# Optimization experiments

Measured on AMD Instinct MI355X. Metric: run time of the kernel, lower is better.

Reference implementation:

```python
import jax, jax.numpy as jnp
import numpy as np

B, T, D, H, K, V, L = 512, 80, 540, 6, 90, 30522, 6  # batch, ctx, d_model, heads, head_size, vocab, blocks


def _layernorm(x, g, b, eps=1e-5):
    m = jnp.mean(x, axis=-1, keepdims=True)
    v = jnp.mean(jnp.square(x - m), axis=-1, keepdims=True)
    return (x - m) * jax.lax.rsqrt(v + eps) * g + b


def setup_inputs() -> dict:
    key = jax.random.key(0)
    ks = jax.random.split(key, 12)
    s = 0.02
    return {
        "x_batch": jax.random.randint(ks[0], (B, T), 0, V),
        "embed": jax.random.normal(ks[1], (V, D), jnp.float32) * s,
        "pos_embed": jax.random.normal(ks[2], (T, D), jnp.float32) * s,
        # per-block stacked per-head projection weights, applied as x @ W
        "Wq": jax.random.normal(ks[3], (L, H, D, K), jnp.float32) * s,
        "Wk": jax.random.normal(ks[4], (L, H, D, K), jnp.float32) * s,
        "Wv": jax.random.normal(ks[5], (L, H, D, K), jnp.float32) * s,
        "W1": jax.random.normal(ks[6], (L, D, H * K), jnp.float32) * s,
        "b1": jnp.zeros((L, H * K), jnp.float32),
        "W2": jax.random.normal(ks[7], (L, H * K, D), jnp.float32) * s,
        "b2": jnp.zeros((L, D), jnp.float32),
        "ln1_g": jnp.ones((L, D), jnp.float32),
        "ln1_b": jnp.zeros((L, D), jnp.float32),
        "ln2_g": jnp.ones((L, D), jnp.float32),
        "ln2_b": jnp.zeros((L, D), jnp.float32),
        "Wc": jax.random.normal(ks[8], (T * D, 1), jnp.float32) * s,
        "bc": jnp.zeros((1,), jnp.float32),
    }


def reference(x_batch, embed, pos_embed, Wq, Wk, Wv, W1, b1, W2, b2,
              ln1_g, ln1_b, ln2_g, ln2_b, Wc, bc):
    x = embed[x_batch] + pos_embed[jnp.arange(x_batch.shape[1])]  # [B,T,D]
    scale = K ** -0.5
    for i in range(L):
        q = jnp.einsum('btd,hdk->bhtk', x, Wq[i])
        k = jnp.einsum('btd,hdk->bhtk', x, Wk[i])
        v = jnp.einsum('btd,hdk->bhtk', x, Wv[i])
        scores = jnp.einsum('btk,bsk->bts'.replace('b', 'bh'), q, k) * scale  # [B,H,T,T]
        # original: Softmax(dim=1) on [B,T,T] -> normalize over the QUERY axis
        attn = jax.nn.softmax(scores, axis=2)
        o = jnp.einsum('bhts,bhsk->bhtk', attn, v)
        o = o.transpose(0, 2, 1, 3).reshape(x.shape)  # concat heads -> [B,T,D]
        x = _layernorm(o + x, ln1_g[i], ln1_b[i])
        ff = jax.nn.relu(x @ W1[i] + b1[i]) @ W2[i] + b2[i]
        x = _layernorm(ff + x, ln2_g[i], ln2_b[i])
    flat = x.reshape(x.shape[0], -1)  # [B, T*D]
    return flat @ Wc + bc  # [B,1]
```

## Files before the change

kernel.cpp:

```cpp
#include <hip/hip_runtime.h>
#include <hip/hip_bf16.h>
#include <math.h>

typedef __hip_bfloat16 bf16;
typedef __bf16 bf16x8 __attribute__((ext_vector_type(8)));
typedef __bf16 bf16x4 __attribute__((ext_vector_type(4)));
typedef float floatx4 __attribute__((ext_vector_type(4)));

#define BB 512
#define TT 80
#define DD 540
#define HH 6
#define KK 90
#define LL 6
#define HK 540
#define N3 1620
#define BT 40960
#define TD 43200
#define KP2 576
#define NQ 1664
#define NQ2 1792
#define NF 640
#define NF2 768
#define TP 104
#define NKT 9

__device__ inline float toF(bf16 x) { return __bfloat162float(x); }


__global__ void prep_wqkv(const float* __restrict__ Wq,
                          const float* __restrict__ Wk,
                          const float* __restrict__ Wv,
                          bf16* __restrict__ wTt) {
    int idx = blockIdx.x * blockDim.x + threadIdx.x;
    const int total = LL * NQ2 * KP2;
    if (idx >= total) return;
    int k = idx % KP2;
    int n = (idx / KP2) % NQ2;
    int l = idx / (KP2 * NQ2);
    float v = 0.f;
    if (k < DD && n < N3) {
        int sel = n / HK;
        int nn = n - sel * HK;
        int h = nn / KK, kk = nn - h * KK;
        const float* W = (sel == 0) ? Wq : ((sel == 1) ? Wk : Wv);
        v = W[(((size_t)l * HH + h) * DD + k) * KK + kk];
    }
    wTt[idx] = __float2bfloat16(v);
}

__global__ void prep_wt(const float* __restrict__ W, bf16* __restrict__ Wt) {
    int idx = blockIdx.x * blockDim.x + threadIdx.x;
    const int total = LL * NF2 * KP2;
    if (idx >= total) return;
    int k = idx % KP2;
    int n = (idx / KP2) % NF2;
    int l = idx / (KP2 * NF2);
    float v = 0.f;
    if (k < DD && n < DD)
        v = W[((size_t)l * DD + k) * DD + n];
    Wt[idx] = __float2bfloat16(v);
}

__global__ void embed_kernel(const int* __restrict__ ids,
                             const float* __restrict__ embed,
                             const float* __restrict__ pos,
                             bf16* __restrict__ xc, int rows) {
    int idx = blockIdx.x * blockDim.x + threadIdx.x;
    int total = rows * KP2;
    if (idx >= total) return;
    int d = idx % KP2;
    int bt = idx / KP2;
    float v = 0.f;
    if (d < DD) {
        int t = bt % TT;
        v = embed[(size_t)ids[bt] * DD + d] + pos[t * DD + d];
    }
    xc[idx] = __float2bfloat16(v);
}


__device__ inline void stage_pair(const bf16* __restrict__ Ab, int lda,
                                  const bf16* __restrict__ Bb,
                                  bf16* ldsbuf, int k0, int wave, int lane,
                                  const int jbase) {
    const int plane = wave >> 1;
    const int kh = plane & 1;
    const bf16* src = (plane < 2) ? Ab : Bb;
    const int ld = (plane < 2) ? lda : KP2;
    const int sc = (lane & 3) ^ ((lane >> 3) & 3);
    const int rsub = lane >> 2;
    bf16* pl = ldsbuf + plane * 8192;
#pragma unroll
    for (int jj = 0; jj < 2; ++jj) {
        int rg = (wave & 1) * 8 + jbase + jj;
        int row = rg * 16 + rsub;
        __builtin_amdgcn_global_load_lds(
            (const __attribute__((address_space(1))) void*)(src + (size_t)row * ld + k0 + kh * 32 + sc * 8),
            (__attribute__((address_space(3))) void*)(pl + rg * 512 + lane * 8), 16, 0, 0);
    }
}

#define READ_A(dst, buf, mh)                                                    \
    _Pragma("unroll")                                                           \
    for (int i_ = 0; i_ < 4; ++i_) {                                            \
        _Pragma("unroll")                                                       \
        for (int kh_ = 0; kh_ < 2; ++kh_) {                                     \
            int row_ = wr * 128 + (4 * (mh) + i_) * 16 + r;                     \
            dst[i_ * 2 + kh_] = *(const bf16x8*)((buf) + kh_ * 8192 + row_ * 32 + ksw); \
        }                                                                       \
    }

#define READ_B(dst, buf, nh)                                                    \
    _Pragma("unroll")                                                           \
    for (int j_ = 0; j_ < 2; ++j_) {                                            \
        _Pragma("unroll")                                                       \
        for (int kh_ = 0; kh_ < 2; ++kh_) {                                     \
            int row_ = wc * 64 + (2 * (nh) + j_) * 16 + r;                      \
            dst[j_ * 2 + kh_] = *(const bf16x8*)((buf) + 16384 + kh_ * 8192 + row_ * 32 + ksw); \
        }                                                                       \
    }

#define MFMA_Q(mh, av, bv, nh)                                                  \
    _Pragma("unroll")                                                           \
    for (int i_ = 0; i_ < 4; ++i_)                                              \
        _Pragma("unroll")                                                       \
        for (int j_ = 0; j_ < 2; ++j_)                                          \
            _Pragma("unroll")                                                   \
            for (int kh_ = 0; kh_ < 2; ++kh_)                                   \
                acc[4 * (mh) + i_][2 * (nh) + j_] =                             \
                    __builtin_amdgcn_mfma_f32_16x16x32_bf16(                    \
                        av[i_ * 2 + kh_], bv[j_ * 2 + kh_],                     \
                        acc[4 * (mh) + i_][2 * (nh) + j_], 0, 0, 0);

#define PHASE_MID                                                               \
    __builtin_amdgcn_s_barrier();                                               \
    asm volatile("s_waitcnt lgkmcnt(0)" ::: "memory");                          \
    __builtin_amdgcn_sched_barrier(0);

#define PHASE_TAIL                                                              \
    __builtin_amdgcn_sched_barrier(0);                                          \
    __builtin_amdgcn_s_barrier();                                               \
    __builtin_amdgcn_sched_barrier(0);

__global__ __launch_bounds__(512, 2) void mfma_gemm2(
    const bf16* __restrict__ A, int lda,
    const bf16* __restrict__ Bt,
    bf16* __restrict__ C, int ldc, int Nreal,
    const float* __restrict__ bias, int relu)
{
    extern __shared__ __align__(16) bf16 ldsb[];
    const int tid = threadIdx.x;
    const int lane = tid & 63;
    const int wave = tid >> 6;
    const int wr = wave >> 2;
    const int wc = wave & 3;
    const int q = lane >> 4, r = lane & 15;

    int bx = blockIdx.x, by = blockIdx.y;
    {
        int nwg = gridDim.x * gridDim.y;
        if ((nwg & 7) == 0) {
            int orig = by * gridDim.x + bx;
            int per = nwg >> 3;
            int swz = (orig & 7) * per + (orig >> 3);
            bx = swz % gridDim.x;
            by = swz / gridDim.x;
        }
    }
    const int row0 = by * 256;
    const int col0 = bx * 256;

    floatx4 acc[8][4];
#pragma unroll
    for (int i = 0; i < 8; ++i)
#pragma unroll
        for (int j = 0; j < 4; ++j) acc[i][j] = (floatx4){0.f, 0.f, 0.f, 0.f};

    const bf16* Ab = A + (size_t)row0 * lda;
    const bf16* Bb = Bt + (size_t)col0 * KP2;

    const int ksw = (q ^ ((r >> 1) & 3)) * 8;

    stage_pair(Ab, lda, Bb, ldsb, 0, wave, lane, 0);
    stage_pair(Ab, lda, Bb, ldsb, 0, wave, lane, 2);
    stage_pair(Ab, lda, Bb, ldsb, 0, wave, lane, 4);
    stage_pair(Ab, lda, Bb, ldsb, 0, wave, lane, 6);
    asm volatile("s_waitcnt vmcnt(0)" ::: "memory");
    __builtin_amdgcn_s_barrier();
    __builtin_amdgcn_sched_barrier(0);

    for (int kt = 0; kt < NKT; ++kt) {
        bf16* buf = ldsb + (kt & 1) * 32768;
        bf16* sbuf = ldsb + ((kt + 1) & 1) * 32768;
        const int k1 = (kt + 1) * 64;
        const bool st = (kt + 1 < NKT);

        bf16x8 a0[8], a1[8], b0[4], b1[4];

        READ_A(a0, buf, 0);
        READ_B(b0, buf, 0);
        if (st) stage_pair(Ab, lda, Bb, sbuf, k1, wave, lane, 0);
        PHASE_MID
        __builtin_amdgcn_s_setprio(1);
        MFMA_Q(0, a0, b0, 0);
        __builtin_amdgcn_s_setprio(0);
        PHASE_TAIL

        READ_A(a1, buf, 1);
        if (st) stage_pair(Ab, lda, Bb, sbuf, k1, wave, lane, 2);
        PHASE_MID
        __builtin_amdgcn_s_setprio(1);
        MFMA_Q(1, a1, b0, 0);
        __builtin_amdgcn_s_setprio(0);
        PHASE_TAIL

        READ_B(b1, buf, 1);
        if (st) stage_pair(Ab, lda, Bb, sbuf, k1, wave, lane, 4);
        PHASE_MID
        __builtin_amdgcn_s_setprio(1);
        MFMA_Q(0, a0, b1, 1);
        __builtin_amdgcn_s_setprio(0);
        PHASE_TAIL

        if (st) stage_pair(Ab, lda, Bb, sbuf, k1, wave, lane, 6);
        PHASE_MID
        __builtin_amdgcn_s_setprio(1);
        MFMA_Q(1, a1, b1, 1);
        __builtin_amdgcn_s_setprio(0);
        asm volatile("s_waitcnt vmcnt(0)" ::: "memory");
        PHASE_TAIL
    }

#pragma unroll
    for (int mi = 0; mi < 8; ++mi) {
        int m0 = row0 + wr * 128 + mi * 16 + q * 4;
#pragma unroll
        for (int ni = 0; ni < 4; ++ni) {
            int n = col0 + wc * 64 + ni * 16 + r;
            if (n < ldc) {
                bool valid = (n < Nreal);
                float bv = (valid && bias) ? bias[n] : 0.f;
#pragma unroll
                for (int reg = 0; reg < 4; ++reg) {
                    float v = acc[mi][ni][reg] + bv;
                    if (relu) v = fmaxf(v, 0.f);
                    if (!valid) v = 0.f;
                    C[(size_t)(m0 + reg) * ldc + n] = __float2bfloat16(v);
                }
            }
        }
    }
}

__global__ __launch_bounds__(320) void attn_mfma(const bf16* __restrict__ qkv,
                                                 bf16* __restrict__ obuf) {
    extern __shared__ bf16 lds[];
    bf16* Qs = lds;
    bf16* Ks = lds + 80 * TP;
    bf16* Vt = lds + 160 * TP;
    const int b = blockIdx.x / HH, h = blockIdx.x % HH;
    const int tid = threadIdx.x;
    const int lane = tid & 63;
    const int w = tid >> 6;
    const int q = lane >> 4, r = lane & 15;
    const bf16* base = qkv + (size_t)b * TT * NQ + h * KK;

    for (int i = tid; i < TT * 12; i += 320) {
        int t = i / 12, kg = i % 12;
        const bf16* qr2 = base + (size_t)t * NQ + kg * 8;
        const bf16* kr2 = qr2 + HK;
        const bf16* vr2 = qr2 + 2 * HK;
        bf16* qd = Qs + t * TP + kg * 8;
        bf16* kd = Ks + t * TP + kg * 8;
#pragma unroll
        for (int j = 0; j < 8; ++j) {
            int k = kg * 8 + j;
            bool ok = (k < KK);
            qd[j] = ok ? qr2[j] : __float2bfloat16(0.f);
            kd[j] = ok ? kr2[j] : __float2bfloat16(0.f);
            Vt[(kg * 8 + j) * TP + t] = ok ? vr2[j] : __float2bfloat16(0.f);
        }
    }
    for (int i = tid; i < 96 * 2; i += 320) {
        int kv = i >> 1, sg = i & 1;
        *(bf16x8*)(Vt + kv * TP + 80 + sg * 8) = (bf16x8)(__bf16)0.0f;
    }
    __syncthreads();

    floatx4 acc[5];
#pragma unroll
    for (int i = 0; i < 5; ++i) acc[i] = (floatx4){0.f, 0.f, 0.f, 0.f};
    bf16x8 bf[3];
#pragma unroll
    for (int ks = 0; ks < 3; ++ks)
        bf[ks] = *(const bf16x8*)(Ks + (16 * w + r) * TP + ks * 32 + q * 8);
#pragma unroll
    for (int ti = 0; ti < 5; ++ti) {
#pragma unroll
        for (int ks = 0; ks < 3; ++ks) {
            bf16x8 af = *(const bf16x8*)(Qs + (16 * ti + r) * TP + ks * 32 + q * 8);
            acc[ti] = __builtin_amdgcn_mfma_f32_16x16x32_bf16(af, bf[ks], acc[ti], 0, 0, 0);
        }
    }

    const float scale = 0.105409255338946f;
    float m = -1e30f;
#pragma unroll
    for (int ti = 0; ti < 5; ++ti)
#pragma unroll
        for (int reg = 0; reg < 4; ++reg) {
            acc[ti][reg] *= scale;
            m = fmaxf(m, acc[ti][reg]);
        }
    m = fmaxf(m, __shfl_xor(m, 16));
    m = fmaxf(m, __shfl_xor(m, 32));
    float sum = 0.f;
    float e[5][4];
#pragma unroll
    for (int ti = 0; ti < 5; ++ti)
#pragma unroll
        for (int reg = 0; reg < 4; ++reg) {
            e[ti][reg] = __expf(acc[ti][reg] - m);
            sum += e[ti][reg];
        }
    sum += __shfl_xor(sum, 16);
    sum += __shfl_xor(sum, 32);
    float inv = 1.f / sum;

    __syncthreads();

    bf16* P = Ks;
#pragma unroll
    for (int ti = 0; ti < 5; ++ti)
#pragma unroll
        for (int reg = 0; reg < 4; ++reg)
            P[(16 * ti + q * 4 + reg) * TP + 16 * w + r] =
                __float2bfloat16(e[ti][reg] * inv);
    for (int i = tid; i < TT * 2; i += 320) {
        int t2 = i >> 1, sg = i & 1;
        *(bf16x8*)(P + t2 * TP + 80 + sg * 8) = (bf16x8)(__bf16)0.0f;
    }
    __syncthreads();

    bf16x8 af2[3];
#pragma unroll
    for (int ks = 0; ks < 3; ++ks)
        af2[ks] = *(const bf16x8*)(P + (16 * w + r) * TP + ks * 32 + q * 8);
    bf16* ob = obuf + ((size_t)b * TT) * NF + h * KK;
#pragma unroll
    for (int nt = 0; nt < 6; ++nt) {
        floatx4 o = (floatx4){0.f, 0.f, 0.f, 0.f};
#pragma unroll
        for (int ks = 0; ks < 3; ++ks) {
            bf16x8 bv = *(const bf16x8*)(Vt + (16 * nt + r) * TP + ks * 32 + q * 8);
            o = __builtin_amdgcn_mfma_f32_16x16x32_bf16(af2[ks], bv, o, 0, 0, 0);
        }
        int kv = 16 * nt + r;
        if (kv < KK) {
#pragma unroll
            for (int reg = 0; reg < 4; ++reg) {
                int t2 = 16 * w + q * 4 + reg;
                ob[(size_t)t2 * NF + kv] = __float2bfloat16(o[reg]);
            }
        }
    }
}

__global__ __launch_bounds__(256) void add_ln_kernel(const bf16* __restrict__ delta,
                                                     bf16* __restrict__ x,
                                                     const float* __restrict__ g,
                                                     const float* __restrict__ bta,
                                                     int nrows) {
    const int w = threadIdx.x >> 6;
    const int lane = threadIdx.x & 63;
    const int row = blockIdx.x * 4 + w;
    if (row >= nrows) return;
    const bf16* dr = delta + (size_t)row * NF;
    bf16* xr = x + (size_t)row * KP2;

    float v[3][4];
    float s1 = 0.f, s2 = 0.f;
#pragma unroll
    for (int s = 0; s < 3; ++s) {
        int c = s * 256 + lane * 4;
        if (c < DD) {
            bf16x4 dv = *(const bf16x4*)(dr + c);
            bf16x4 xv = *(const bf16x4*)(xr + c);
#pragma unroll
            for (int j = 0; j < 4; ++j) {
                float t = (float)dv[j] + (float)xv[j];
                v[s][j] = t;
                s1 += t; s2 += t * t;
            }
        } else {
#pragma unroll
            for (int j = 0; j < 4; ++j) v[s][j] = 0.f;
        }
    }
#pragma unroll
    for (int o = 32; o > 0; o >>= 1) {
        s1 += __shfl_xor(s1, o, 64);
        s2 += __shfl_xor(s2, o, 64);
    }
    const float mean = s1 * (1.f / DD);
    const float var = s2 * (1.f / DD) - mean * mean;
    const float rstd = rsqrtf(var + 1e-5f);
#pragma unroll
    for (int s = 0; s < 3; ++s) {
        int c = s * 256 + lane * 4;
        if (c < DD) {
            float4 gv = *(const float4*)(g + c);
            float4 bv = *(const float4*)(bta + c);
            bf16x4 ov;
            ov[0] = (__bf16)((v[s][0] - mean) * rstd * gv.x + bv.x);
            ov[1] = (__bf16)((v[s][1] - mean) * rstd * gv.y + bv.y);
            ov[2] = (__bf16)((v[s][2] - mean) * rstd * gv.z + bv.z);
            ov[3] = (__bf16)((v[s][3] - mean) * rstd * gv.w + bv.w);
            *(bf16x4*)(xr + c) = ov;
        }
    }
}

__global__ __launch_bounds__(256) void final_kernel(const bf16* __restrict__ xc,
                                                    const float* __restrict__ Wc,
                                                    const float* __restrict__ bc,
                                                    float* __restrict__ out) {
    int b = blockIdx.x;
    int tid = threadIdx.x;
    const bf16* xb = xc + (size_t)b * TT * KP2;
    float s = 0.f;
    for (int i = tid; i < TD; i += 256) {
        int t = i / DD, d = i - t * DD;
        s += toF(xb[(size_t)t * KP2 + d]) * Wc[i];
    }
    for (int o = 32; o > 0; o >>= 1) s += __shfl_down(s, o, 64);
    __shared__ float red[4];
    int lane = tid & 63, w = tid >> 6;
    if (lane == 0) red[w] = s;
    __syncthreads();
    if (tid == 0) out[b] = red[0] + red[1] + red[2] + red[3] + bc[0];
}

extern "C" void kernel_launch(void* const* d_in, const int* in_sizes, int n_in,
                              void* d_out, int out_size, void* d_ws, size_t ws_size,
                              hipStream_t stream) {
    const int* ids    = (const int*)d_in[0];
    const float* embed = (const float*)d_in[1];
    const float* pos  = (const float*)d_in[2];
    const float* Wq   = (const float*)d_in[3];
    const float* Wk   = (const float*)d_in[4];
    const float* Wv   = (const float*)d_in[5];
    const float* W1   = (const float*)d_in[6];
    const float* b1   = (const float*)d_in[7];
    const float* W2   = (const float*)d_in[8];
    const float* b2   = (const float*)d_in[9];
    const float* ln1g = (const float*)d_in[10];
    const float* ln1b = (const float*)d_in[11];
    const float* ln2g = (const float*)d_in[12];
    const float* ln2b = (const float*)d_in[13];
    const float* Wc   = (const float*)d_in[14];
    const float* bc   = (const float*)d_in[15];
    float* out = (float*)d_out;

    const size_t wqkvB = (size_t)LL * NQ2 * KP2 * 2;
    const size_t wffB  = (size_t)LL * NF2 * KP2 * 2;
    const size_t fixed = wqkvB + 2 * wffB;
    const size_t perB  = (size_t)TT * 2 * (KP2 + NQ + NF);

    int bch = BB;
    while (bch > 16 && fixed + (size_t)bch * perB > ws_size) bch >>= 1;
    int nch = BB / bch;
    int rows = bch * TT;

    char* p = (char*)d_ws;
    bf16* wTt = (bf16*)p;  p += wqkvB;
    bf16* W1t = (bf16*)p;  p += wffB;
    bf16* W2t = (bf16*)p;  p += wffB;
    bf16* xc  = (bf16*)p;  p += (size_t)rows * KP2 * 2;
    bf16* scr = (bf16*)p;  p += (size_t)rows * NQ * 2;
    bf16* dch = (bf16*)p;

    prep_wqkv<<<(LL * NQ2 * KP2 + 255) / 256, 256, 0, stream>>>(Wq, Wk, Wv, wTt);
    prep_wt<<<(LL * NF2 * KP2 + 255) / 256, 256, 0, stream>>>(W1, W1t);
    prep_wt<<<(LL * NF2 * KP2 + 255) / 256, 256, 0, stream>>>(W2, W2t);

    dim3 gq(NQ2 / 256, rows / 256);
    dim3 gf(NF2 / 256, rows / 256);
    const size_t gemm_lds = 2 * 32768 * sizeof(bf16);
    const size_t attn_lds = (size_t)(160 + 96) * TP * 2;
    const int lnGrid = (rows + 3) / 4;

    for (int c = 0; c < nch; ++c) {
        embed_kernel<<<(rows * KP2 + 255) / 256, 256, 0, stream>>>(
            ids + (size_t)c * rows, embed, pos, xc, rows);
        for (int l = 0; l < LL; ++l) {
            mfma_gemm2<<<gq, 512, gemm_lds, stream>>>(
                xc, KP2, wTt + (size_t)l * NQ2 * KP2, scr, NQ, N3,
                (const float*)nullptr, 0);
            attn_mfma<<<bch * HH, 320, attn_lds, stream>>>(scr, dch);
            add_ln_kernel<<<lnGrid, 256, 0, stream>>>(dch, xc, ln1g + l * DD, ln1b + l * DD, rows);
            mfma_gemm2<<<gf, 512, gemm_lds, stream>>>(
                xc, KP2, W1t + (size_t)l * NF2 * KP2, scr, NF, HK,
                b1 + (size_t)l * HK, 1);
            mfma_gemm2<<<gf, 512, gemm_lds, stream>>>(
                scr, NF, W2t + (size_t)l * NF2 * KP2, dch, NF, DD,
                b2 + (size_t)l * DD, 0);
            add_ln_kernel<<<lnGrid, 256, 0, stream>>>(dch, xc, ln2g + l * DD, ln2b + l * DD, rows);
        }
        final_kernel<<<bch, 256, 0, stream>>>(xc, Wc, bc, out + (size_t)c * bch);
    }
}
```

Baseline: 2.465 ms.

## Pad QKV heads to 96 columns and simplify GEMM staging to whole-tile prefetch

The fused QKV weight layout now pads each head from 90 to 96 columns. The attention kernel can then load Q, K and V rows with aligned 16-byte vector loads instead of per-element guarded copies. Separately, the GEMM main loop drops its four-phase interleaved staging with intra-iteration barriers. It now issues the full next-tile prefetch at loop start, reads all LDS fragments, runs all MFMAs, and syncs once per k-step. This cuts barrier overhead and scalar attention loads, at the cost of a slightly wider QKV output and less fine-grained overlap of global loads with compute.

```diff
diff --git a/kernel.cpp b/kernel.cpp
--- a/kernel.cpp
+++ b/kernel.cpp
@@ -14,11 +14,12 @@
 #define KK 90
 #define LL 6
 #define HK 540
-#define N3 1620
+#define KKA 96
+#define HKA 576
+#define NQA 1728
 #define BT 40960
 #define TD 43200
 #define KP2 576
-#define NQ 1664
 #define NQ2 1792
 #define NF 640
 #define NF2 768
@@ -39,12 +40,14 @@
     int n = (idx / KP2) % NQ2;
     int l = idx / (KP2 * NQ2);
     float v = 0.f;
-    if (k < DD && n < N3) {
-        int sel = n / HK;
-        int nn = n - sel * HK;
-        int h = nn / KK, kk = nn - h * KK;
-        const float* W = (sel == 0) ? Wq : ((sel == 1) ? Wk : Wv);
-        v = W[(((size_t)l * HH + h) * DD + k) * KK + kk];
+    if (k < DD && n < NQA) {
+        int sel = n / HKA;
+        int nn = n - sel * HKA;
+        int h = nn / KKA, kk = nn - h * KKA;
+        if (kk < KK) {
+            const float* W = (sel == 0) ? Wq : ((sel == 1) ? Wk : Wv);
+            v = W[(((size_t)l * HH + h) * DD + k) * KK + kk];
+        }
     }
     wTt[idx] = __float2bfloat16(v);
 }
@@ -80,10 +83,9 @@
 }
 
 
-__device__ inline void stage_pair(const bf16* __restrict__ Ab, int lda,
-                                  const bf16* __restrict__ Bb,
-                                  bf16* ldsbuf, int k0, int wave, int lane,
-                                  const int jbase) {
+__device__ inline void stage_tile8(const bf16* __restrict__ Ab, int lda,
+                                   const bf16* __restrict__ Bb,
+                                   bf16* ldsbuf, int k0, int wave, int lane) {
     const int plane = wave >> 1;
     const int kh = plane & 1;
     const bf16* src = (plane < 2) ? Ab : Bb;
@@ -92,8 +94,8 @@
     const int rsub = lane >> 2;
     bf16* pl = ldsbuf + plane * 8192;
 #pragma unroll
-    for (int jj = 0; jj < 2; ++jj) {
-        int rg = (wave & 1) * 8 + jbase + jj;
+    for (int jj = 0; jj < 8; ++jj) {
+        int rg = (wave & 1) * 8 + jj;
         int row = rg * 16 + rsub;
         __builtin_amdgcn_global_load_lds(
             (const __attribute__((address_space(1))) void*)(src + (size_t)row * ld + k0 + kh * 32 + sc * 8),
@@ -132,16 +134,6 @@
                     __builtin_amdgcn_mfma_f32_16x16x32_bf16(                    \
                         av[i_ * 2 + kh_], bv[j_ * 2 + kh_],                     \
                         acc[4 * (mh) + i_][2 * (nh) + j_], 0, 0, 0);
-
-#define PHASE_MID                                                               \
-    __builtin_amdgcn_s_barrier();                                               \
-    asm volatile("s_waitcnt lgkmcnt(0)" ::: "memory");                          \
-    __builtin_amdgcn_sched_barrier(0);
-
-#define PHASE_TAIL                                                              \
-    __builtin_amdgcn_sched_barrier(0);                                          \
-    __builtin_amdgcn_s_barrier();                                               \
-    __builtin_amdgcn_sched_barrier(0);
 
 __global__ __launch_bounds__(512, 2) void mfma_gemm2(
     const bf16* __restrict__ A, int lda,
@@ -182,54 +174,36 @@
 
     const int ksw = (q ^ ((r >> 1) & 3)) * 8;
 
-    stage_pair(Ab, lda, Bb, ldsb, 0, wave, lane, 0);
-    stage_pair(Ab, lda, Bb, ldsb, 0, wave, lane, 2);
-    stage_pair(Ab, lda, Bb, ldsb, 0, wave, lane, 4);
-    stage_pair(Ab, lda, Bb, ldsb, 0, wave, lane, 6);
+    stage_tile8(Ab, lda, Bb, ldsb, 0, wave, lane);
     asm volatile("s_waitcnt vmcnt(0)" ::: "memory");
+    __builtin_amdgcn_sched_barrier(0);
     __builtin_amdgcn_s_barrier();
     __builtin_amdgcn_sched_barrier(0);
 
     for (int kt = 0; kt < NKT; ++kt) {
-        bf16* buf = ldsb + (kt & 1) * 32768;
+        bf16* buf  = ldsb + (kt & 1) * 32768;
         bf16* sbuf = ldsb + ((kt + 1) & 1) * 32768;
-        const int k1 = (kt + 1) * 64;
-        const bool st = (kt + 1 < NKT);
+
+        if (kt + 1 < NKT)
+            stage_tile8(Ab, lda, Bb, sbuf, (kt + 1) * 64, wave, lane);
 
         bf16x8 a0[8], a1[8], b0[4], b1[4];
-
         READ_A(a0, buf, 0);
         READ_B(b0, buf, 0);
-        if (st) stage_pair(Ab, lda, Bb, sbuf, k1, wave, lane, 0);
-        PHASE_MID
+        READ_A(a1, buf, 1);
+        READ_B(b1, buf, 1);
+
         __builtin_amdgcn_s_setprio(1);
         MFMA_Q(0, a0, b0, 0);
-        __builtin_amdgcn_s_setprio(0);
-        PHASE_TAIL
-
-        READ_A(a1, buf, 1);
-        if (st) stage_pair(Ab, lda, Bb, sbuf, k1, wave, lane, 2);
-        PHASE_MID
-        __builtin_amdgcn_s_setprio(1);
         MFMA_Q(1, a1, b0, 0);
-        __builtin_amdgcn_s_setprio(0);
-        PHASE_TAIL
-
-        READ_B(b1, buf, 1);
-        if (st) stage_pair(Ab, lda, Bb, sbuf, k1, wave, lane, 4);
-        PHASE_MID
-        __builtin_amdgcn_s_setprio(1);
         MFMA_Q(0, a0, b1, 1);
-        __builtin_amdgcn_s_setprio(0);
-        PHASE_TAIL
-
-        if (st) stage_pair(Ab, lda, Bb, sbuf, k1, wave, lane, 6);
-        PHASE_MID
-        __builtin_amdgcn_s_setprio(1);
         MFMA_Q(1, a1, b1, 1);
         __builtin_amdgcn_s_setprio(0);
+
         asm volatile("s_waitcnt vmcnt(0)" ::: "memory");
-        PHASE_TAIL
+        __builtin_amdgcn_sched_barrier(0);
+        __builtin_amdgcn_s_barrier();
+        __builtin_amdgcn_sched_barrier(0);
     }
 
 #pragma unroll
@@ -259,28 +233,25 @@
     bf16* Qs = lds;
     bf16* Ks = lds + 80 * TP;
     bf16* Vt = lds + 160 * TP;
+    __bf16* Vtb = (__bf16*)Vt;
     const int b = blockIdx.x / HH, h = blockIdx.x % HH;
     const int tid = threadIdx.x;
     const int lane = tid & 63;
     const int w = tid >> 6;
     const int q = lane >> 4, r = lane & 15;
-    const bf16* base = qkv + (size_t)b * TT * NQ + h * KK;
+    const bf16* base = qkv + (size_t)b * TT * NQA + h * KKA;
 
     for (int i = tid; i < TT * 12; i += 320) {
         int t = i / 12, kg = i % 12;
-        const bf16* qr2 = base + (size_t)t * NQ + kg * 8;
-        const bf16* kr2 = qr2 + HK;
-        const bf16* vr2 = qr2 + 2 * HK;
-        bf16* qd = Qs + t * TP + kg * 8;
-        bf16* kd = Ks + t * TP + kg * 8;
-#pragma unroll
-        for (int j = 0; j < 8; ++j) {
-            int k = kg * 8 + j;
-            bool ok = (k < KK);
-            qd[j] = ok ? qr2[j] : __float2bfloat16(0.f);
-            kd[j] = ok ? kr2[j] : __float2bfloat16(0.f);
-            Vt[(kg * 8 + j) * TP + t] = ok ? vr2[j] : __float2bfloat16(0.f);
-        }
+        const bf16* qr2 = base + (size_t)t * NQA + kg * 8;
+        bf16x8 qv = *(const bf16x8*)qr2;
+        bf16x8 kv2 = *(const bf16x8*)(qr2 + HKA);
+        bf16x8 vv = *(const bf16x8*)(qr2 + 2 * HKA);
+        *(bf16x8*)(Qs + t * TP + kg * 8) = qv;
+        *(bf16x8*)(Ks + t * TP + kg * 8) = kv2;
+#pragma unroll
+        for (int j = 0; j < 8; ++j)
+            Vtb[(kg * 8 + j) * TP + t] = vv[j];
     }
     for (int i = tid; i < 96 * 2; i += 320) {
         int kv = i >> 1, sg = i & 1;
@@ -466,7 +437,7 @@
     const size_t wqkvB = (size_t)LL * NQ2 * KP2 * 2;
     const size_t wffB  = (size_t)LL * NF2 * KP2 * 2;
     const size_t fixed = wqkvB + 2 * wffB;
-    const size_t perB  = (size_t)TT * 2 * (KP2 + NQ + NF);
+    const size_t perB  = (size_t)TT * 2 * (KP2 + NQA + NF);
 
     int bch = BB;
     while (bch > 16 && fixed + (size_t)bch * perB > ws_size) bch >>= 1;
@@ -478,7 +449,7 @@
     bf16* W1t = (bf16*)p;  p += wffB;
     bf16* W2t = (bf16*)p;  p += wffB;
     bf16* xc  = (bf16*)p;  p += (size_t)rows * KP2 * 2;
-    bf16* scr = (bf16*)p;  p += (size_t)rows * NQ * 2;
+    bf16* scr = (bf16*)p;  p += (size_t)rows * NQA * 2;
     bf16* dch = (bf16*)p;
 
     prep_wqkv<<<(LL * NQ2 * KP2 + 255) / 256, 256, 0, stream>>>(Wq, Wk, Wv, wTt);
@@ -496,7 +467,7 @@
             ids + (size_t)c * rows, embed, pos, xc, rows);
         for (int l = 0; l < LL; ++l) {
             mfma_gemm2<<<gq, 512, gemm_lds, stream>>>(
-                xc, KP2, wTt + (size_t)l * NQ2 * KP2, scr, NQ, N3,
+                xc, KP2, wTt + (size_t)l * NQ2 * KP2, scr, NQA, NQA,
                 (const float*)nullptr, 0);
             attn_mfma<<<bch * HH, 320, attn_lds, stream>>>(scr, dch);
             add_ln_kernel<<<lnGrid, 256, 0, stream>>>(dch, xc, ln1g + l * DD, ln1b + l * DD, rows);
```

After: 2.138 ms. 13.3% less time.
